# Kernel tuning notes

Hardware: AMD Instinct MI355X
Metric: run time of the kernel (lower is better)

Reference implementation:

```python
import jax, jax.numpy as jnp
import numpy as np

RADIUS = 0.1
NSAMPLE = 32


def setup_inputs() -> dict:
    key = jax.random.key(0)
    k1, k2, k3, k4, k5 = jax.random.split(key, 5)
    B, NPOINT, N, C = 4, 2048, 8192, 64
    query_xyz = jax.random.uniform(k1, (B, 3, NPOINT), dtype=jnp.float32)
    support_xyz = jax.random.uniform(k2, (B, 3, N), dtype=jnp.float32)
    query_mask = jax.random.bernoulli(k3, 0.9, (B, NPOINT))
    support_mask = jax.random.bernoulli(k4, 0.9, (B, N))
    features = jax.random.normal(k5, (B, C, N), dtype=jnp.float32)
    return {"query_xyz": query_xyz, "support_xyz": support_xyz,
            "query_mask": query_mask, "support_mask": support_mask,
            "features": features}


def _masked_ordered_ball_query(query_xyz, support_xyz, query_mask, support_mask,
                               radius, nsample):
    # query_xyz: (B,3,npoint), support_xyz: (B,3,N)
    q = query_xyz.transpose(0, 2, 1)    # (B, npoint, 3)
    s = support_xyz.transpose(0, 2, 1)  # (B, N, 3)
    N = s.shape[1]
    # squared pairwise distances via |q|^2 + |s|^2 - 2 q.s  -> (B, npoint, N)
    d2 = (jnp.sum(q * q, -1)[:, :, None]
          + jnp.sum(s * s, -1)[:, None, :]
          - 2.0 * jnp.einsum('bpd,bnd->bpn', q, s))
    within = (d2 <= radius * radius) \
        & support_mask[:, None, :] & query_mask[:, :, None]
    # ordered selection of the first `nsample` in-ball indices (ascending index)
    score = jnp.where(within, N - jnp.arange(N, dtype=jnp.int32), 0)
    vals, idx = jax.lax.top_k(score, nsample)     # (B, npoint, nsample)
    idx_mask = vals > 0                            # true neighbors
    # pad slots with the first found neighbor (0 if none found)
    first = jnp.where(idx_mask[..., :1], idx[..., :1], 0)
    idx = jnp.where(idx_mask, idx, first)
    return idx, idx_mask


def _group(points_nc, idx):
    # points_nc: (B, N, D), idx: (B, npoint, nsample) -> (B, npoint, nsample, D)
    return jax.vmap(lambda p, i: p[i])(points_nc, idx)


def reference(query_xyz, support_xyz, query_mask, support_mask, features):
    idx, idx_mask = _masked_ordered_ball_query(
        query_xyz, support_xyz, query_mask, support_mask, RADIUS, NSAMPLE)
    s = support_xyz.transpose(0, 2, 1)             # (B, N, 3)
    grouped_xyz = _group(s, idx).transpose(0, 3, 1, 2)   # (B,3,npoint,nsample)
    grouped_xyz = grouped_xyz - query_xyz[:, :, :, None]
    grouped_xyz = grouped_xyz / RADIUS             # normalize_xyz=True
    f = features.transpose(0, 2, 1)                # (B, N, C)
    grouped_features = _group(f, idx).transpose(0, 3, 1, 2)  # (B,C,npoint,nsample)
    new_features = jnp.concatenate([grouped_xyz, grouped_features], axis=1)
    return new_features, idx_mask
```

## Files before the change

kernel.cpp:

```cpp
#include <hip/hip_runtime.h>


#define NPOINT 2048
#define NSUP   8192
#define NCH    64
#define NS     32
#define GRID1  10
#define CELLS  1000
#define QCHUNK 1024

__device__ __forceinline__ bool probe_mask4(const void* mask) {
    const unsigned char* mb = (const unsigned char*)mask;
    const int lane = threadIdx.x & 63;
    return __ballot(mb[4 * lane + 1] != 0) == 0ull;
}
__device__ __forceinline__ bool read_mask(const void* mask, int i, bool is4) {
    return is4 ? (((const int*)mask)[i] != 0)
               : (((const unsigned char*)mask)[i] != 0);
}
__device__ __forceinline__ int cell_of(float x, float y, float z) {
    const int cx = min(GRID1 - 1, (int)(x * 10.0f));
    const int cy = min(GRID1 - 1, (int)(y * 10.0f));
    const int cz = min(GRID1 - 1, (int)(z * 10.0f));
    return cx + GRID1 * cy + GRID1 * GRID1 * cz;
}

__global__ __launch_bounds__(1024) void build_grid(
    const float* __restrict__ support_xyz, const void* __restrict__ support_mask,
    int* __restrict__ starts, float4* __restrict__ pts)
{
    __shared__ int hist[CELLS];
    __shared__ int scanb[CELLS];
    __shared__ int cur[CELLS];
    __shared__ int wavesum[16];
    const int b    = blockIdx.x;
    const int tid  = threadIdx.x;
    const int wid  = tid >> 6;
    const int lane = tid & 63;
    const bool m4 = probe_mask4(support_mask);
    const float* sx = support_xyz + (size_t)b * 3 * NSUP;

    if (tid < CELLS) { hist[tid] = 0; cur[tid] = 0; }
    __syncthreads();

    float xr[8], yr[8], zr[8]; int cidr[8]; bool mr[8];
    #pragma unroll
    for (int i = 0; i < 8; ++i) {
        const int n = tid + 1024 * i;
        xr[i] = sx[n];
        yr[i] = sx[NSUP + n];
        zr[i] = sx[2 * NSUP + n];
        mr[i] = read_mask(support_mask, b * NSUP + n, m4);
        cidr[i] = cell_of(xr[i], yr[i], zr[i]);
        if (mr[i]) atomicAdd(&hist[cidr[i]], 1);
    }
    __syncthreads();

    int v = (tid < CELLS) ? hist[tid] : 0;
    #pragma unroll
    for (int d = 1; d < 64; d <<= 1) {
        const int u = __shfl_up(v, d, 64);
        if (lane >= d) v += u;
    }
    if (lane == 63) wavesum[wid] = v;
    __syncthreads();
    if (wid == 0) {
        int w = (lane < 16) ? wavesum[lane] : 0;
        #pragma unroll
        for (int d = 1; d < 16; d <<= 1) {
            const int u = __shfl_up(w, d, 64);
            if (lane >= d) w += u;
        }
        if (lane < 16) wavesum[lane] = w;
    }
    __syncthreads();
    if (wid > 0) v += wavesum[wid - 1];
    int* stg = starts + b * (CELLS + 1);
    if (tid == 0) stg[0] = 0;
    if (tid < CELLS) { stg[tid + 1] = v; scanb[tid] = v; }
    __syncthreads();

    #pragma unroll
    for (int i = 0; i < 8; ++i) {
        if (mr[i]) {
            const int c    = cidr[i];
            const int base = (c == 0) ? 0 : scanb[c - 1];
            const int pos  = base + atomicAdd(&cur[c], 1);
            pts[(size_t)b * NSUP + pos] =
                make_float4(xr[i], yr[i], zr[i], __int_as_float(tid + 1024 * i));
        }
    }
}

__global__ __launch_bounds__(256) void mqag_query(
    const float* __restrict__ query_xyz, const float* __restrict__ support_xyz,
    const void* __restrict__ query_mask, const void* __restrict__ support_mask,
    const float4* __restrict__ pts, const int* __restrict__ starts,
    int* __restrict__ idx_ws, float* __restrict__ out, int B)
{
#pragma clang fp contract(off)
    const int wib  = threadIdx.x >> 6;
    const int lane = threadIdx.x & 63;
    const int qid  = blockIdx.x * 4 + wib;
    const int b    = qid / NPOINT;
    const int p    = qid % NPOINT;

    __shared__ int hits_all[4][64];
    __shared__ int slots_all[4][NS];
    int* hits  = hits_all[wib];
    int* slots = slots_all[wib];

    const bool m4q = probe_mask4(query_mask);

    const float* sx = support_xyz + (size_t)b * 3 * NSUP;
    const float* sy = sx + NSUP;
    const float* sz = sx + 2 * NSUP;

    const float qx = query_xyz[(size_t)b * 3 * NPOINT + p];
    const float qy = query_xyz[(size_t)b * 3 * NPOINT + NPOINT + p];
    const float qz = query_xyz[(size_t)b * 3 * NPOINT + 2 * NPOINT + p];
    const bool  qm = read_mask(query_mask, b * NPOINT + p, m4q);
    const float qq = (qx * qx + qy * qy) + qz * qz;

    int T = 0;
    int eT[16], aT[16];
    if (qm) {
        const int x0 = max(0, (int)floorf((qx - 0.101f) * 10.f));
        const int x1 = min(GRID1 - 1, (int)floorf((qx + 0.101f) * 10.f));
        const int y0 = max(0, (int)floorf((qy - 0.101f) * 10.f));
        const int y1 = min(GRID1 - 1, (int)floorf((qy + 0.101f) * 10.f));
        const int z0 = max(0, (int)floorf((qz - 0.101f) * 10.f));
        const int z1 = min(GRID1 - 1, (int)floorf((qz + 0.101f) * 10.f));
        const int* stb = starts + b * (CELLS + 1);

        const int jz = lane >> 2, jy = lane & 3;
        const int cz = z0 + jz,  cy = y0 + jy;
        bool act = (lane < 16) && (cz <= z1) && (cy <= y1);
        int len = 0, s0 = 0;
        if (act) {
            const float cyl = cy * 0.1f, czl = cz * 0.1f;
            const float dy = fmaxf(0.0f, fmaxf(cyl - qy, qy - (cyl + 0.1f)));
            const float dz = fmaxf(0.0f, fmaxf(czl - qz, qz - (czl + 0.1f)));
            const float rem = 0.0101f - (dy * dy + dz * dz);
            if (rem < 0.0f) {
                act = false;
            } else {
                const float mx = sqrtf(rem);
                const int x0r = max(x0, (int)floorf((qx - mx - 0.0005f) * 10.f));
                const int x1r = min(x1, (int)floorf((qx + mx + 0.0005f) * 10.f));
                const int c0 = x0r + GRID1 * cy + GRID1 * GRID1 * cz;
                s0  = stb[c0];
                len = stb[c0 + (x1r - x0r + 1)] - s0;
            }
        }
        if (!act) { len = 0; s0 = 0; }
        int pre = len;
        #pragma unroll
        for (int d = 1; d < 16; d <<= 1) {
            const int v = __shfl_up(pre, d, 64);
            if (lane >= d) pre += v;
        }
        const int adj = s0 - (pre - len);
        #pragma unroll
        for (int j = 0; j < 16; ++j) {
            eT[j] = __builtin_amdgcn_readlane(pre, j);
            aT[j] = __builtin_amdgcn_readlane(adj, j);
        }
        T = eT[15];
    }

    const float4* ptsb = pts + (size_t)b * NSUP;
    auto resolve = [&](int g) {
        int adjv = 0;
        #pragma unroll
        for (int j = 15; j >= 0; --j)
            if (g < eT[j]) adjv = aT[j];
        return g + adjv;
    };
    int cnt = 0;
    float4 pv;
    if (T > 0) pv = ptsb[(lane < T) ? resolve(lane) : 0];
    for (int tb = 0; tb < T; tb += 64) {
        float4 nx;
        const int tb2 = tb + 64;
        if (tb2 < T) {
            const int gn = tb2 + lane;
            nx = ptsb[(gn < T) ? resolve(gn) : 0];
        }
        const bool valid = (tb + lane) < T;
        const int nidx = __float_as_int(pv.w);
        const float ss  = (pv.x * pv.x + pv.y * pv.y) + pv.z * pv.z;
        const float dot = __builtin_fmaf(qz, pv.z,
                          __builtin_fmaf(qy, pv.y, qx * pv.x));
        const float d2  = (qq + ss) - 2.0f * dot;
        const bool within = valid && (d2 <= 0.01f);
        const unsigned long long bal = __ballot(within);
        if (within) {
            const int r = cnt + __popcll(bal & ((1ull << lane) - 1ull));
            if (r < 64) hits[r] = nidx;
        }
        cnt += __popcll(bal);
        pv = nx;
    }

    if (cnt > 64) {
        const bool m4s = probe_mask4(support_mask);
        int c2 = 0;
        for (int basei = 0; basei < NSUP; basei += 64) {
            const int n = basei + lane;
            const float x = sx[n], y = sy[n], z = sz[n];
            const bool  m = read_mask(support_mask, b * NSUP + n, m4s);
            const float ss  = (x * x + y * y) + z * z;
            const float dot = __builtin_fmaf(qz, z,
                              __builtin_fmaf(qy, y, qx * x));
            const float d2  = (qq + ss) - 2.0f * dot;
            const bool within = (d2 <= 0.01f) && m;
            const unsigned long long bal = __ballot(within);
            if (within) {
                const int r = c2 + __popcll(bal & ((1ull << lane) - 1ull));
                if (r < NS) slots[r] = n;
            }
            c2 += __popcll(bal);
            if (c2 >= NS) break;
        }
        cnt = c2;
    } else {
        int v = (lane < cnt) ? hits[lane] : 0x7FFFFFFF;
        #pragma unroll
        for (int k = 2; k <= 64; k <<= 1) {
            #pragma unroll
            for (int j = k >> 1; j > 0; j >>= 1) {
                const int pv2 = __shfl_xor(v, j, 64);
                const bool keep_min = ((lane & j) == 0) == ((lane & k) == 0);
                const int mn = min(v, pv2), mx = max(v, pv2);
                v = keep_min ? mn : mx;
            }
        }
        if (lane < NS && lane < cnt) slots[lane] = v;
    }
    const int found = (cnt < NS) ? cnt : NS;

    const int first = (found > 0) ? slots[0] : 0;
    if (lane < NS && lane >= found) slots[lane] = first;

    if (lane < NS) idx_ws[((size_t)b * NPOINT + p) * NS + lane] = slots[lane];

    const size_t nf_elems = (size_t)B * 67 * NPOINT * NS;
    if (lane < NS) {
        out[nf_elems + ((size_t)b * NPOINT + p) * NS + lane] =
            (lane < found) ? 1.0f : 0.0f;
    }

    for (int i = 0; i < 2; ++i) {
        const int flat = i * 64 + lane;
        if (flat < 3 * NS) {
            const int ch = flat >> 5;
            const int k  = flat & 31;
            const int idx = slots[k];
            const float s = sx[(size_t)ch * NSUP + idx];
            const float q = (ch == 0) ? qx : ((ch == 1) ? qy : qz);
            out[(((size_t)b * 67 + ch) * NPOINT + p) * NS + k] = (s - q) / 0.1f;
        }
    }
}

__global__ __launch_bounds__(256) void gather_feat(
    const float* __restrict__ features, const int* __restrict__ idx_ws,
    float* __restrict__ out, int B)
{
    __shared__ float row[NSUP];
    const int bc = blockIdx.y;
    const int b  = bc / NCH, ch = bc % NCH;
    const int p0 = blockIdx.x * QCHUNK;

    const float* src = features + ((size_t)b * NCH + ch) * NSUP;
    const float4* src4 = (const float4*)src;
    for (int i = threadIdx.x; i < NSUP / 4; i += 256)
        ((float4*)row)[i] = src4[i];
    __syncthreads();

    const int4* idx4 = (const int4*)(idx_ws + ((size_t)b * NPOINT + p0) * NS);
    float4* dst4 = (float4*)(out + (((size_t)b * 67 + 3 + ch) * NPOINT + p0) * NS);
    for (int e = threadIdx.x; e < QCHUNK * NS / 4; e += 256) {
        const int4 iv = idx4[e];
        dst4[e] = make_float4(row[iv.x], row[iv.y], row[iv.z], row[iv.w]);
    }
}

__global__ __launch_bounds__(256) void mqag_linear(
    const float* __restrict__ query_xyz, const float* __restrict__ support_xyz,
    const void* __restrict__ query_mask_raw, const void* __restrict__ support_mask_raw,
    const float* __restrict__ features, float* __restrict__ out, int B)
{
#pragma clang fp contract(off)
    const int wib  = threadIdx.x >> 6;
    const int lane = threadIdx.x & 63;
    const int qid  = blockIdx.x * 4 + wib;
    const int b    = qid / NPOINT;
    const int p    = qid % NPOINT;

    __shared__ int slots_all[4][NS];
    int* slots = slots_all[wib];

    const bool m4s = probe_mask4(support_mask_raw);
    const bool m4q = probe_mask4(query_mask_raw);

    const float* sx = support_xyz + (size_t)b * 3 * NSUP;
    const float* sy = sx + NSUP;
    const float* sz = sx + 2 * NSUP;

    const float qx = query_xyz[(size_t)b * 3 * NPOINT + p];
    const float qy = query_xyz[(size_t)b * 3 * NPOINT + NPOINT + p];
    const float qz = query_xyz[(size_t)b * 3 * NPOINT + 2 * NPOINT + p];
    const bool  qm = read_mask(query_mask_raw, b * NPOINT + p, m4q);
    const float qq = (qx * qx + qy * qy) + qz * qz;

    int cnt = 0;
    if (qm) {
        for (int base = 0; base < NSUP; base += 64) {
            const int n = base + lane;
            const float x = sx[n], y = sy[n], z = sz[n];
            const bool  m = read_mask(support_mask_raw, b * NSUP + n, m4s);
            const float ss  = (x * x + y * y) + z * z;
            const float dot = __builtin_fmaf(qz, z, __builtin_fmaf(qy, y, qx * x));
            const float d2  = (qq + ss) - 2.0f * dot;
            const bool within = (d2 <= 0.01f) && m;
            const unsigned long long bal = __ballot(within);
            if (within) {
                const int r = cnt + __popcll(bal & ((1ull << lane) - 1ull));
                if (r < NS) slots[r] = n;
            }
            cnt += __popcll(bal);
            if (cnt >= NS) break;
        }
    }
    const int found = cnt < NS ? cnt : NS;
    __syncthreads();
    const int first = (found > 0) ? slots[0] : 0;
    if (lane < NS && lane >= found) slots[lane] = first;
    __syncthreads();

    const size_t nf_elems = (size_t)B * 67 * NPOINT * NS;
    if (lane < NS) {
        out[nf_elems + ((size_t)b * NPOINT + p) * NS + lane] =
            (lane < found) ? 1.0f : 0.0f;
    }
    const float* feat = features + (size_t)b * NCH * NSUP;
    for (int i = 0; i < (67 * NS + 63) / 64; ++i) {
        const int flat = i * 64 + lane;
        if (flat < 67 * NS) {
            const int ch = flat >> 5;
            const int k  = flat & 31;
            const int idx = slots[k];
            float val;
            if (ch < 3) {
                const float s = sx[(size_t)ch * NSUP + idx];
                const float q = (ch == 0) ? qx : ((ch == 1) ? qy : qz);
                val = (s - q) / 0.1f;
            } else {
                val = feat[(size_t)(ch - 3) * NSUP + idx];
            }
            out[(((size_t)b * 67 + ch) * NPOINT + p) * NS + k] = val;
        }
    }
}

extern "C" void kernel_launch(void* const* d_in, const int* in_sizes, int n_in,
                              void* d_out, int out_size, void* d_ws, size_t ws_size,
                              hipStream_t stream) {
    const float* query_xyz    = (const float*)d_in[0];
    const float* support_xyz  = (const float*)d_in[1];
    const void*  query_mask   = d_in[2];
    const void*  support_mask = d_in[3];
    const float* features     = (const float*)d_in[4];

    const int B = in_sizes[0] / (3 * NPOINT);

    const size_t off_pts    = 0;
    const size_t off_starts = off_pts + (size_t)B * NSUP * sizeof(float4);
    const size_t off_idx    = off_starts + (size_t)B * (CELLS + 1) * sizeof(int);
    const size_t need = off_idx + (size_t)B * NPOINT * NS * sizeof(int);

    if (ws_size >= need) {
        float4* pts  = (float4*)((char*)d_ws + off_pts);
        int* starts  = (int*)((char*)d_ws + off_starts);
        int* idx_ws  = (int*)((char*)d_ws + off_idx);

        hipLaunchKernelGGL(build_grid, dim3(B), dim3(1024), 0, stream,
                           support_xyz, support_mask, starts, pts);
        hipLaunchKernelGGL(mqag_query, dim3(B * NPOINT / 4), dim3(256), 0,
                           stream, query_xyz, support_xyz, query_mask,
                           support_mask, pts, starts, idx_ws, (float*)d_out, B);
        hipLaunchKernelGGL(gather_feat, dim3(NPOINT / QCHUNK, B * NCH), dim3(256),
                           0, stream, features, idx_ws, (float*)d_out, B);
    } else {
        hipLaunchKernelGGL(mqag_linear, dim3(B * NPOINT / 4), dim3(256), 0,
                           stream, query_xyz, support_xyz, query_mask,
                           support_mask, features, (float*)d_out, B);
    }
}
```

Before: 114.6 us.

## Vectorize grid-build loads, parallelize cell bounds, and widen feature gather

build_grid now loads eight contiguous xyz values and mask entries per thread with vector loads and packs the mask bits, so the original index mapping changes to tid*8+i. mqag_query fetches cell start and end offsets in separate lanes and combines them with a shuffle, replacing two dependent loads per lane. gather_feat processes all 2048 points per (batch, channel) in one 512-thread block, so each feature row is staged into shared memory once, and it uses nontemporal loads and stores. In exchange the gather grid shrinks to 256 blocks, which may leave fewer blocks in flight.

```diff
diff --git a/kernel.cpp b/kernel.cpp
--- a/kernel.cpp
+++ b/kernel.cpp
@@ -7,7 +7,9 @@
 #define NS     32
 #define GRID1  10
 #define CELLS  1000
-#define QCHUNK 1024
+#define QCHUNK 2048
+
+typedef float nvec4 __attribute__((ext_vector_type(4)));
 
 __device__ __forceinline__ bool probe_mask4(const void* mask) {
     const unsigned char* mb = (const unsigned char*)mask;
@@ -43,16 +45,38 @@
     if (tid < CELLS) { hist[tid] = 0; cur[tid] = 0; }
     __syncthreads();
 
-    float xr[8], yr[8], zr[8]; int cidr[8]; bool mr[8];
+    const float4* x4 = (const float4*)sx;
+    const float4* y4 = (const float4*)(sx + NSUP);
+    const float4* z4 = (const float4*)(sx + 2 * NSUP);
+    const float4 xa = x4[tid * 2], xb = x4[tid * 2 + 1];
+    const float4 ya = y4[tid * 2], yb = y4[tid * 2 + 1];
+    const float4 za = z4[tid * 2], zb = z4[tid * 2 + 1];
+    unsigned mk;
+    if (m4) {
+        const int4* mi4 = (const int4*)((const int*)support_mask + (size_t)b * NSUP);
+        const int4 ma = mi4[tid * 2], mb2 = mi4[tid * 2 + 1];
+        mk = (ma.x  != 0 ? 1u   : 0u) | (ma.y  != 0 ? 2u   : 0u)
+           | (ma.z  != 0 ? 4u   : 0u) | (ma.w  != 0 ? 8u   : 0u)
+           | (mb2.x != 0 ? 16u  : 0u) | (mb2.y != 0 ? 32u  : 0u)
+           | (mb2.z != 0 ? 64u  : 0u) | (mb2.w != 0 ? 128u : 0u);
+    } else {
+        const unsigned char* mb = (const unsigned char*)support_mask
+                                + (size_t)b * NSUP + (size_t)tid * 8;
+        const unsigned lo = *(const unsigned*)(mb);
+        const unsigned hi = *(const unsigned*)(mb + 4);
+        mk = ((lo & 0xffu)        ? 1u   : 0u) | ((lo & 0xff00u)     ? 2u   : 0u)
+           | ((lo & 0xff0000u)    ? 4u   : 0u) | ((lo & 0xff000000u) ? 8u   : 0u)
+           | ((hi & 0xffu)        ? 16u  : 0u) | ((hi & 0xff00u)     ? 32u  : 0u)
+           | ((hi & 0xff0000u)    ? 64u  : 0u) | ((hi & 0xff000000u) ? 128u : 0u);
+    }
+    const float xr[8] = {xa.x, xa.y, xa.z, xa.w, xb.x, xb.y, xb.z, xb.w};
+    const float yr[8] = {ya.x, ya.y, ya.z, ya.w, yb.x, yb.y, yb.z, yb.w};
+    const float zr[8] = {za.x, za.y, za.z, za.w, zb.x, zb.y, zb.z, zb.w};
+    int cidr[8];
     #pragma unroll
     for (int i = 0; i < 8; ++i) {
-        const int n = tid + 1024 * i;
-        xr[i] = sx[n];
-        yr[i] = sx[NSUP + n];
-        zr[i] = sx[2 * NSUP + n];
-        mr[i] = read_mask(support_mask, b * NSUP + n, m4);
         cidr[i] = cell_of(xr[i], yr[i], zr[i]);
-        if (mr[i]) atomicAdd(&hist[cidr[i]], 1);
+        if ((mk >> i) & 1u) atomicAdd(&hist[cidr[i]], 1);
     }
     __syncthreads();
 
@@ -82,12 +106,12 @@
 
     #pragma unroll
     for (int i = 0; i < 8; ++i) {
-        if (mr[i]) {
+        if ((mk >> i) & 1u) {
             const int c    = cidr[i];
             const int base = (c == 0) ? 0 : scanb[c - 1];
             const int pos  = base + atomicAdd(&cur[c], 1);
             pts[(size_t)b * NSUP + pos] =
-                make_float4(xr[i], yr[i], zr[i], __int_as_float(tid + 1024 * i));
+                make_float4(xr[i], yr[i], zr[i], __int_as_float(tid * 8 + i));
         }
     }
 }
@@ -133,10 +157,11 @@
         const int z1 = min(GRID1 - 1, (int)floorf((qz + 0.101f) * 10.f));
         const int* stb = starts + b * (CELLS + 1);
 
-        const int jz = lane >> 2, jy = lane & 3;
+        const int j  = lane & 15;
+        const int jz = j >> 2, jy = j & 3;
         const int cz = z0 + jz,  cy = y0 + jy;
-        bool act = (lane < 16) && (cz <= z1) && (cy <= y1);
-        int len = 0, s0 = 0;
+        bool act = (lane < 32) && (cz <= z1) && (cy <= y1);
+        int sval = 0;
         if (act) {
             const float cyl = cy * 0.1f, czl = cz * 0.1f;
             const float dy = fmaxf(0.0f, fmaxf(cyl - qy, qy - (cyl + 0.1f)));
@@ -149,11 +174,13 @@
                 const int x0r = max(x0, (int)floorf((qx - mx - 0.0005f) * 10.f));
                 const int x1r = min(x1, (int)floorf((qx + mx + 0.0005f) * 10.f));
                 const int c0 = x0r + GRID1 * cy + GRID1 * GRID1 * cz;
-                s0  = stb[c0];
-                len = stb[c0 + (x1r - x0r + 1)] - s0;
+                sval = (lane < 16) ? stb[c0] : stb[c0 + (x1r - x0r + 1)];
             }
         }
-        if (!act) { len = 0; s0 = 0; }
+        if (!act) sval = 0;
+        const int endv = __shfl(sval, (lane & 15) + 16, 64);
+        const int s0   = sval;
+        int len = (lane < 16 && act) ? (endv - s0) : 0;
         int pre = len;
         #pragma unroll
         for (int d = 1; d < 16; d <<= 1) {
@@ -162,9 +189,9 @@
         }
         const int adj = s0 - (pre - len);
         #pragma unroll
-        for (int j = 0; j < 16; ++j) {
-            eT[j] = __builtin_amdgcn_readlane(pre, j);
-            aT[j] = __builtin_amdgcn_readlane(adj, j);
+        for (int jj = 0; jj < 16; ++jj) {
+            eT[jj] = __builtin_amdgcn_readlane(pre, jj);
+            aT[jj] = __builtin_amdgcn_readlane(adj, jj);
         }
         T = eT[15];
     }
@@ -173,8 +200,8 @@
     auto resolve = [&](int g) {
         int adjv = 0;
         #pragma unroll
-        for (int j = 15; j >= 0; --j)
-            if (g < eT[j]) adjv = aT[j];
+        for (int jj = 15; jj >= 0; --jj)
+            if (g < eT[jj]) adjv = aT[jj];
         return g + adjv;
     };
     int cnt = 0;
@@ -229,9 +256,9 @@
         #pragma unroll
         for (int k = 2; k <= 64; k <<= 1) {
             #pragma unroll
-            for (int j = k >> 1; j > 0; j >>= 1) {
-                const int pv2 = __shfl_xor(v, j, 64);
-                const bool keep_min = ((lane & j) == 0) == ((lane & k) == 0);
+            for (int j2 = k >> 1; j2 > 0; j2 >>= 1) {
+                const int pv2 = __shfl_xor(v, j2, 64);
+                const bool keep_min = ((lane & j2) == 0) == ((lane & k) == 0);
                 const int mn = min(v, pv2), mx = max(v, pv2);
                 v = keep_min ? mn : mx;
             }
@@ -264,26 +291,27 @@
     }
 }
 
-__global__ __launch_bounds__(256) void gather_feat(
+__global__ __launch_bounds__(512) void gather_feat(
     const float* __restrict__ features, const int* __restrict__ idx_ws,
     float* __restrict__ out, int B)
 {
     __shared__ float row[NSUP];
     const int bc = blockIdx.y;
     const int b  = bc / NCH, ch = bc % NCH;
-    const int p0 = blockIdx.x * QCHUNK;
 
     const float* src = features + ((size_t)b * NCH + ch) * NSUP;
-    const float4* src4 = (const float4*)src;
-    for (int i = threadIdx.x; i < NSUP / 4; i += 256)
-        ((float4*)row)[i] = src4[i];
-    __syncthreads();
-
-    const int4* idx4 = (const int4*)(idx_ws + ((size_t)b * NPOINT + p0) * NS);
-    float4* dst4 = (float4*)(out + (((size_t)b * 67 + 3 + ch) * NPOINT + p0) * NS);
-    for (int e = threadIdx.x; e < QCHUNK * NS / 4; e += 256) {
+    const nvec4* src4 = (const nvec4*)src;
+    for (int i = threadIdx.x; i < NSUP / 4; i += 512)
+        ((nvec4*)row)[i] = __builtin_nontemporal_load(&src4[i]);
+    __syncthreads();
+
+    const int4* idx4 = (const int4*)(idx_ws + ((size_t)b * NPOINT) * NS);
+    nvec4* dst4 = (nvec4*)(out + (((size_t)b * 67 + 3 + ch) * NPOINT) * NS);
+    for (int e = threadIdx.x; e < QCHUNK * NS / 4; e += 512) {
         const int4 iv = idx4[e];
-        dst4[e] = make_float4(row[iv.x], row[iv.y], row[iv.z], row[iv.w]);
+        nvec4 g;
+        g.x = row[iv.x]; g.y = row[iv.y]; g.z = row[iv.z]; g.w = row[iv.w];
+        __builtin_nontemporal_store(g, &dst4[e]);
     }
 }
 
@@ -391,7 +419,7 @@
         hipLaunchKernelGGL(mqag_query, dim3(B * NPOINT / 4), dim3(256), 0,
                            stream, query_xyz, support_xyz, query_mask,
                            support_mask, pts, starts, idx_ws, (float*)d_out, B);
-        hipLaunchKernelGGL(gather_feat, dim3(NPOINT / QCHUNK, B * NCH), dim3(256),
+        hipLaunchKernelGGL(gather_feat, dim3(1, B * NCH), dim3(512),
                            0, stream, features, idx_ws, (float*)d_out, B);
     } else {
         hipLaunchKernelGGL(mqag_linear, dim3(B * NPOINT / 4), dim3(256), 0,
```

New measurement: 118.1 us. 1.03x slower.
